# Kernel optimization log

Measured on AMD Instinct MI355X. Metric: run time of the kernel, lower is better.

The kernel has to match this reference:

```python
import jax, jax.numpy as jnp
import numpy as np

EMBED_DIM = 1024
NUM_HEADS = 16
HEAD_DIM = EMBED_DIM // NUM_HEADS
SCALE = HEAD_DIM ** -0.5


def setup_inputs() -> dict:
    key = jax.random.key(0)
    ks = jax.random.split(key, 5)
    B, N, D = 8, 1024, EMBED_DIM
    std = D ** -0.5
    x = jax.random.normal(ks[0], (B, N, D), dtype=jnp.float32)
    W_qkv = jax.random.normal(ks[1], (D, 3 * D), dtype=jnp.float32) * std
    b_qkv = jnp.zeros((3 * D,), dtype=jnp.float32)
    W_proj = jax.random.normal(ks[2], (D, D), dtype=jnp.float32) * std
    b_proj = jnp.zeros((D,), dtype=jnp.float32)
    return {"x": x, "W_qkv": W_qkv, "b_qkv": b_qkv, "W_proj": W_proj, "b_proj": b_proj}


def reference(x, W_qkv, b_qkv, W_proj, b_proj):
    B, N, D = x.shape
    H, hd = NUM_HEADS, HEAD_DIM
    # QKV projection: (B,N,3D) -> (3,B,H,N,hd)
    qkv = (x @ W_qkv + b_qkv).reshape(B, N, 3, H, hd).transpose(2, 0, 3, 1, 4)
    q, k, v = qkv[0], qkv[1], qkv[2]
    # scaled dot-product attention, full (B,H,N,N) scores as in original
    attn = jnp.einsum('bhqd,bhkd->bhqk', q, k) * SCALE
    attn = jax.nn.softmax(attn, axis=-1)
    out = jnp.einsum('bhqk,bhkd->bhqd', attn, v)  # (B,H,N,hd)
    out = out.transpose(0, 2, 1, 3).reshape(B, N, D)
    return out @ W_proj + b_proj
```

## Files before the change

### kernel.cpp

```cpp
#include <hip/hip_runtime.h>

#define AS1(p) ((const __attribute__((address_space(1))) void*)(p))
#define AS3(p) ((__attribute__((address_space(3))) void*)(p))

typedef __attribute__((ext_vector_type(8))) short bf16x8;
typedef __attribute__((ext_vector_type(4))) float f32x4;
typedef __attribute__((ext_vector_type(16))) float f32x16;

static constexpr int kBatch = 8;
static constexpr int kSeq = 1024;
static constexpr int kD = 1024;
static constexpr int kH = 16;
static constexpr int kHD = 64;
static constexpr int kRows = kBatch * kSeq;
static constexpr int kQKVCols = 3 * kD;

__device__ __forceinline__ unsigned short f2bf(float f) {
  union { float f; unsigned int u; } a; a.f = f;
  unsigned int r = a.u + 0x7fffu + ((a.u >> 16) & 1u);
  return (unsigned short)(r >> 16);
}

__device__ __forceinline__ unsigned pkbf(float a, float b) {
  unsigned r;
  asm("v_cvt_pk_bf16_f32 %0, %1, %2" : "=v"(r) : "v"(a), "v"(b));
  return r;
}

__global__ void cvt_bf16_kernel(const float* __restrict__ in,
                                unsigned short* __restrict__ out, int n4) {
  int i = blockIdx.x * blockDim.x + threadIdx.x;
  int stride = gridDim.x * blockDim.x;
  for (; i < n4; i += stride) {
    float4 v = reinterpret_cast<const float4*>(in)[i];
    ushort4 o;
    o.x = f2bf(v.x); o.y = f2bf(v.y); o.z = f2bf(v.z); o.w = f2bf(v.w);
    reinterpret_cast<ushort4*>(out)[i] = o;
  }
}

__global__ void transpose_cvt_kernel(const float* __restrict__ W,
                                     unsigned short* __restrict__ Wt,
                                     int rows, int cols) {
  __shared__ float tile[32][33];
  int c0 = blockIdx.x * 32, r0 = blockIdx.y * 32;
  int tx = threadIdx.x, ty = threadIdx.y;
#pragma unroll
  for (int i = 0; i < 32; i += 8)
    tile[ty + i][tx] = W[(size_t)(r0 + ty + i) * cols + (c0 + tx)];
  __syncthreads();
#pragma unroll
  for (int i = 0; i < 32; i += 8)
    Wt[(size_t)(c0 + ty + i) * rows + (r0 + tx)] = f2bf(tile[tx][ty + i]);
}

__device__ __forceinline__ int swap23(int x) {
  return (x & ~12) | ((x & 4) << 1) | ((x & 8) >> 1);
}
__global__ __launch_bounds__(256) void vtrans_kernel(
    const unsigned short* __restrict__ qkv, unsigned short* __restrict__ Vt) {
  __shared__ alignas(16) unsigned short tile[64][72];
  const int nt = blockIdx.x, bh = blockIdx.y;
  const int b = bh >> 4, h = bh & 15;
  const unsigned short* Vb = qkv + (size_t)b * kSeq * kQKVCols + 2 * kD + h * kHD;
  const int t = threadIdx.x;
#pragma unroll
  for (int r = 0; r < 2; ++r) {
    const int c = r * 256 + t;
    const int n = c >> 3, d8 = c & 7;
    uint4 v = *reinterpret_cast<const uint4*>(Vb + (size_t)(nt * 64 + n) * kQKVCols + d8 * 8);
    *reinterpret_cast<uint4*>(&tile[n][d8 * 8]) = v;
  }
  __syncthreads();
#pragma unroll
  for (int r = 0; r < 2; ++r) {
    const int c = r * 256 + t;
    const int d = c >> 3, n8 = c & 7;
    unsigned short w8[8];
#pragma unroll
    for (int j = 0; j < 8; ++j) w8[j] = tile[swap23(n8 * 8 + j)][d];
    *reinterpret_cast<uint4*>(Vt + (size_t)bh * kHD * kSeq + (size_t)d * kSeq + nt * 64 + n8 * 8) =
        *reinterpret_cast<uint4*>(w8);
  }
}

template <bool OUT_BF16>
__global__ __launch_bounds__(256) void gemm_bt_kernel(
    const unsigned short* __restrict__ A,
    const unsigned short* __restrict__ Bt,
    const float* __restrict__ bias,
    void* __restrict__ Cout, int M, int Nn, int K) {
  constexpr int BK = 64;
  __shared__ alignas(16) unsigned short As[128 * BK];
  __shared__ alignas(16) unsigned short Bs[128 * BK];
  const int t = threadIdx.x;
  const int lane = t & 63;
  const int w = t >> 6;
  const int wr = w >> 1, wc = w & 1;
  const int l15 = lane & 15, lhi = lane >> 4;
  const int nwg = gridDim.x * gridDim.y;
  const int lin = blockIdx.y * gridDim.x + blockIdx.x;
  const int swz = (lin & 7) * (nwg >> 3) + (lin >> 3);
  const int row0 = (swz / gridDim.x) * 128;
  const int col0 = (swz % gridDim.x) * 128;

  f32x4 acc[4][4] = {};
  const int ldsb = (t & ~63) * 16;

  for (int k0 = 0; k0 < K; k0 += BK) {
    __syncthreads();
#pragma unroll
    for (int r = 0; r < 4; ++r) {
      int c = r * 256 + t;
      int arow = c >> 3;
      int ccol = ((c & 7) ^ (arow & 7)) * 8;
      const unsigned short* ga = A + (size_t)(row0 + arow) * K + (k0 + ccol);
      const unsigned short* gb = Bt + (size_t)(col0 + arow) * K + (k0 + ccol);
      char* la = (char*)As + r * 4096 + ldsb;
      char* lb = (char*)Bs + r * 4096 + ldsb;
      __builtin_amdgcn_global_load_lds(AS1(ga), AS3(la), 16, 0, 0);
      __builtin_amdgcn_global_load_lds(AS1(gb), AS3(lb), 16, 0, 0);
    }
    __syncthreads();
#pragma unroll
    for (int kk = 0; kk < 2; ++kk) {
      bf16x8 af[4], bfr[4];
#pragma unroll
      for (int mi = 0; mi < 4; ++mi) {
        int rowa = wr * 64 + mi * 16 + l15;
        int chunk = (kk * 4 + lhi) ^ (rowa & 7);
        af[mi] = *reinterpret_cast<const bf16x8*>((const char*)As + rowa * 128 + chunk * 16);
      }
#pragma unroll
      for (int ni = 0; ni < 4; ++ni) {
        int rowb = wc * 64 + ni * 16 + l15;
        int chunk = (kk * 4 + lhi) ^ (rowb & 7);
        bfr[ni] = *reinterpret_cast<const bf16x8*>((const char*)Bs + rowb * 128 + chunk * 16);
      }
#pragma unroll
      for (int mi = 0; mi < 4; ++mi)
#pragma unroll
        for (int ni = 0; ni < 4; ++ni)
          acc[mi][ni] = __builtin_amdgcn_mfma_f32_16x16x32_bf16(af[mi], bfr[ni], acc[mi][ni], 0, 0, 0);
    }
  }
#pragma unroll
  for (int mi = 0; mi < 4; ++mi) {
    int rbase = row0 + wr * 64 + mi * 16 + lhi * 4;
#pragma unroll
    for (int ni = 0; ni < 4; ++ni) {
      int col = col0 + wc * 64 + ni * 16 + l15;
      float bv = bias[col];
#pragma unroll
      for (int j = 0; j < 4; ++j) {
        float v = acc[mi][ni][j] + bv;
        if (OUT_BF16)
          ((unsigned short*)Cout)[(size_t)(rbase + j) * Nn + col] = f2bf(v);
        else
          ((float*)Cout)[(size_t)(rbase + j) * Nn + col] = v;
      }
    }
  }
}

__global__ __launch_bounds__(256) void attn_kernel(
    const unsigned short* __restrict__ qkv,
    const unsigned short* __restrict__ Vt,
    unsigned short* __restrict__ ctx) {
  __shared__ alignas(16) char smem[32768];
  const int qt = blockIdx.x >> 7;
  const int bh = blockIdx.x & 127;
  const int b = bh >> 4, h = bh & 15;
  const int t = threadIdx.x, lane = t & 63, w = t >> 6;
  const int l31 = lane & 31, hi = lane >> 5;

  const unsigned short* Qb = qkv + (size_t)b * kSeq * kQKVCols + h * kHD;
  const unsigned short* Kb = Qb + kD;
  const unsigned short* Vtb = Vt + (size_t)bh * kHD * kSeq;

  bf16x8 qf[4];
  const int qrow = qt * 128 + w * 32 + l31;
#pragma unroll
  for (int s = 0; s < 4; ++s)
    qf[s] = *reinterpret_cast<const bf16x8*>(Qb + (size_t)qrow * kQKVCols + s * 16 + hi * 8);

  auto stage = [&](int kt, int bufb) {
#pragma unroll
    for (int r = 0; r < 2; ++r) {
      const int c = r * 256 + t;
      const int row = c >> 3;
      const int sc = ((c & 7) ^ (row & 7)) * 8;
      const unsigned short* gk = Kb + (size_t)(kt * 64 + row) * kQKVCols + sc;
      const unsigned short* gv = Vtb + (size_t)row * kSeq + kt * 64 + sc;
      char* lk = smem + bufb + r * 4096 + (t & ~63) * 16;
      char* lv = smem + bufb + 8192 + r * 4096 + (t & ~63) * 16;
      __builtin_amdgcn_global_load_lds(AS1(gk), AS3(lk), 16, 0, 0);
      __builtin_amdgcn_global_load_lds(AS1(gv), AS3(lv), 16, 0, 0);
    }
  };

  f32x16 oacc[2] = {};
  float mrun = -3.0e38f, lrun = 0.f;
  constexpr float kSc = 0.125f * 1.44269504f;

  stage(0, 0);
  __syncthreads();
  int cur = 0;
  for (int kt = 0; kt < 16; ++kt) {
    if (kt < 15) stage(kt + 1, (cur ^ 1) * 16384);
    const char* Kp = smem + cur * 16384;
    const char* Vp = Kp + 8192;

    f32x16 sacc[2] = {};
    __builtin_amdgcn_s_setprio(1);
#pragma unroll
    for (int nb = 0; nb < 2; ++nb) {
      const int n = nb * 32 + l31;
#pragma unroll
      for (int s = 0; s < 4; ++s) {
        const int ch = (s * 2 + hi) ^ (n & 7);
        bf16x8 kf = *reinterpret_cast<const bf16x8*>(Kp + n * 128 + ch * 16);
        sacc[nb] = __builtin_amdgcn_mfma_f32_32x32x16_bf16(kf, qf[s], sacc[nb], 0, 0, 0);
      }
    }
    __builtin_amdgcn_s_setprio(0);

    float tm = sacc[0][0];
#pragma unroll
    for (int nb = 0; nb < 2; ++nb)
#pragma unroll
      for (int r = 0; r < 16; ++r) tm = fmaxf(tm, sacc[nb][r]);
    tm = fmaxf(tm, __shfl_xor(tm, 32, 64));
    const float tms = tm * kSc;
    if (!__all(tms <= mrun + 8.0f)) {
      const float mnew = fmaxf(mrun, tms);
      const float corr = __builtin_amdgcn_exp2f(mrun - mnew);
      mrun = mnew;
      lrun *= corr;
#pragma unroll
      for (int db = 0; db < 2; ++db)
#pragma unroll
        for (int r = 0; r < 16; ++r) oacc[db][r] *= corr;
    }
    float ps = 0.f;
#pragma unroll
    for (int nb = 0; nb < 2; ++nb)
#pragma unroll
      for (int r = 0; r < 16; ++r) {
        const float e = __builtin_amdgcn_exp2f(__builtin_fmaf(sacc[nb][r], kSc, -mrun));
        sacc[nb][r] = e;
        ps += e;
      }
    lrun += ps + __shfl_xor(ps, 32, 64);

    bf16x8 pf[4];
#pragma unroll
    for (int s = 0; s < 4; ++s) {
      const int nb = s >> 1, h2 = (s & 1) * 8;
      union { unsigned u[4]; bf16x8 v; } pk4;
#pragma unroll
      for (int i = 0; i < 4; ++i)
        pk4.u[i] = pkbf(sacc[nb][h2 + 2 * i], sacc[nb][h2 + 2 * i + 1]);
      pf[s] = pk4.v;
    }

    __builtin_amdgcn_s_setprio(1);
#pragma unroll
    for (int db = 0; db < 2; ++db) {
      const int dr = db * 32 + l31;
#pragma unroll
      for (int s = 0; s < 4; ++s) {
        const int ch = (s * 2 + hi) ^ (dr & 7);
        bf16x8 vf = *reinterpret_cast<const bf16x8*>(Vp + dr * 128 + ch * 16);
        oacc[db] = __builtin_amdgcn_mfma_f32_32x32x16_bf16(vf, pf[s], oacc[db], 0, 0, 0);
      }
    }
    __builtin_amdgcn_s_setprio(0);
    __syncthreads();
    cur ^= 1;
  }

  const float rl = 1.0f / lrun;
  const int qlocal = w * 32 + l31;
#pragma unroll
  for (int db = 0; db < 2; ++db)
#pragma unroll
    for (int g = 0; g < 4; ++g) {
      const unsigned u0 = pkbf(oacc[db][g * 4 + 0] * rl, oacc[db][g * 4 + 1] * rl);
      const unsigned u1 = pkbf(oacc[db][g * 4 + 2] * rl, oacc[db][g * 4 + 3] * rl);
      const int ch = db * 4 + g;
      uint2 uu; uu.x = u0; uu.y = u1;
      *reinterpret_cast<uint2*>(smem + qlocal * 128 + ((ch ^ (qlocal & 7)) * 16) + hi * 8) = uu;
    }
  __syncthreads();
#pragma unroll
  for (int it = 0; it < 4; ++it) {
    const int idx = it * 256 + t;
    const int row = idx >> 3, ch = idx & 7;
    const uint4 vv = *reinterpret_cast<const uint4*>(smem + row * 128 + ((ch ^ (row & 7)) * 16));
    *reinterpret_cast<uint4*>(ctx + (size_t)(b * kSeq + qt * 128 + row) * kD + h * kHD + ch * 8) = vv;
  }
}

extern "C" void kernel_launch(void* const* d_in, const int* in_sizes, int n_in,
                              void* d_out, int out_size, void* d_ws, size_t ws_size,
                              hipStream_t stream) {
  const float* x     = (const float*)d_in[0];
  const float* Wqkv  = (const float*)d_in[1];
  const float* bqkv  = (const float*)d_in[2];
  const float* Wproj = (const float*)d_in[3];
  const float* bproj = (const float*)d_in[4];
  float* out = (float*)d_out;

  char* ws = (char*)d_ws;
  size_t oXbf   = 0;
  size_t oWqkvT = oXbf   + (size_t)kRows * kD * 2;
  size_t oWpT   = oWqkvT + (size_t)kQKVCols * kD * 2;
  size_t oQKV   = oWpT   + (size_t)kD * kD * 2;
  size_t oCTX   = oQKV   + (size_t)kRows * kQKVCols * 2;
  size_t total  = oCTX   + (size_t)kRows * kD * 2;
  if (ws_size < total) return;

  unsigned short* Xbf   = (unsigned short*)(ws + oXbf);
  unsigned short* Vtb   = (unsigned short*)(ws + oXbf);
  unsigned short* WqkvT = (unsigned short*)(ws + oWqkvT);
  unsigned short* WpT   = (unsigned short*)(ws + oWpT);
  unsigned short* QKV   = (unsigned short*)(ws + oQKV);
  unsigned short* CTX   = (unsigned short*)(ws + oCTX);

  cvt_bf16_kernel<<<2048, 256, 0, stream>>>(x, Xbf, kRows * kD / 4);
  transpose_cvt_kernel<<<dim3(kQKVCols / 32, kD / 32), dim3(32, 8), 0, stream>>>(Wqkv, WqkvT, kD, kQKVCols);
  transpose_cvt_kernel<<<dim3(kD / 32, kD / 32), dim3(32, 8), 0, stream>>>(Wproj, WpT, kD, kD);
  gemm_bt_kernel<true><<<dim3(kQKVCols / 128, kRows / 128), 256, 0, stream>>>(
      Xbf, WqkvT, bqkv, QKV, kRows, kQKVCols, kD);
  vtrans_kernel<<<dim3(16, 128), 256, 0, stream>>>(QKV, Vtb);
  attn_kernel<<<1024, 256, 0, stream>>>(QKV, Vtb, CTX);
  gemm_bt_kernel<false><<<dim3(kD / 128, kRows / 128), 256, 0, stream>>>(
      CTX, WpT, bproj, out, kRows, kD, kD);
}
```

Baseline: 168.8 us.

## Add 256x256-tile 8-wave pipelined GEMM for QKV projection

Result: no change. 170.1 us (+0.8%).

```diff
diff --git a/kernel.cpp b/kernel.cpp
--- a/kernel.cpp
+++ b/kernel.cpp
@@ -163,6 +163,137 @@
   }
 }
 
+#define G256_STAGE_A(BUF, HALF, KT)                                           \
+  do {                                                                        \
+    char* _d = smem + (BUF) * 65536 + (HALF) * 16384 + ldst;                  \
+    const unsigned short* _s0 = Ap + aoff0 + (size_t)(HALF) * halfstep + (KT) * 64; \
+    const unsigned short* _s1 = Ap + aoff1 + (size_t)(HALF) * halfstep + (KT) * 64; \
+    __builtin_amdgcn_global_load_lds(AS1(_s0), AS3(_d), 16, 0, 0);            \
+    __builtin_amdgcn_global_load_lds(AS1(_s1), AS3(_d + 8192), 16, 0, 0);     \
+  } while (0)
+#define G256_STAGE_B(BUF, HALF, KT)                                           \
+  do {                                                                        \
+    char* _d = smem + (BUF) * 65536 + 32768 + (HALF) * 16384 + ldst;          \
+    const unsigned short* _s0 = Bp + boff0 + (size_t)(HALF) * halfstep + (KT) * 64; \
+    const unsigned short* _s1 = Bp + boff1 + (size_t)(HALF) * halfstep + (KT) * 64; \
+    __builtin_amdgcn_global_load_lds(AS1(_s0), AS3(_d), 16, 0, 0);            \
+    __builtin_amdgcn_global_load_lds(AS1(_s1), AS3(_d + 8192), 16, 0, 0);     \
+  } while (0)
+#define G256_PHASE(RBUF, QM, QN, STAGE_STMT, DO_VM)                           \
+  do {                                                                        \
+    const char* _Ab = smem + (RBUF) * 65536 + (QM) * 16384;                   \
+    const char* _Bb = smem + (RBUF) * 65536 + 32768 + (QN) * 16384;           \
+    bf16x8 _af[2][4], _bf[2][2];                                              \
+    _Pragma("unroll") for (int kk = 0; kk < 2; ++kk) {                        \
+      _Pragma("unroll") for (int mi = 0; mi < 4; ++mi) {                      \
+        const int rr = wm * 64 + mi * 16 + l15;                               \
+        const int ch = (kk * 4 + lhi) ^ (rr & 7);                             \
+        _af[kk][mi] = *reinterpret_cast<const bf16x8*>(_Ab + rr * 128 + ch * 16); \
+      }                                                                       \
+      _Pragma("unroll") for (int ni = 0; ni < 2; ++ni) {                      \
+        const int rr = wn * 32 + ni * 16 + l15;                               \
+        const int ch = (kk * 4 + lhi) ^ (rr & 7);                             \
+        _bf[kk][ni] = *reinterpret_cast<const bf16x8*>(_Bb + rr * 128 + ch * 16); \
+      }                                                                       \
+    }                                                                         \
+    STAGE_STMT;                                                               \
+    if (DO_VM) asm volatile("s_waitcnt vmcnt(4)" ::: "memory");               \
+    asm volatile("" ::: "memory");                                            \
+    __builtin_amdgcn_s_barrier();                                             \
+    asm volatile("s_waitcnt lgkmcnt(0)" ::: "memory");                        \
+    __builtin_amdgcn_sched_barrier(0);                                        \
+    __builtin_amdgcn_s_setprio(1);                                            \
+    _Pragma("unroll") for (int kk = 0; kk < 2; ++kk)                          \
+      _Pragma("unroll") for (int mi = 0; mi < 4; ++mi)                        \
+        _Pragma("unroll") for (int ni = 0; ni < 2; ++ni)                      \
+          acc[QM][QN][mi][ni] = __builtin_amdgcn_mfma_f32_16x16x32_bf16(      \
+              _af[kk][mi], _bf[kk][ni], acc[QM][QN][mi][ni], 0, 0, 0);        \
+    __builtin_amdgcn_s_setprio(0);                                            \
+    asm volatile("" ::: "memory");                                            \
+    __builtin_amdgcn_s_barrier();                                             \
+    asm volatile("" ::: "memory");                                            \
+  } while (0)
+
+template <bool OUT_BF16>
+__global__ __launch_bounds__(512, 2) void gemm256_kernel(
+    const unsigned short* __restrict__ Ap,
+    const unsigned short* __restrict__ Bp,
+    const float* __restrict__ bias,
+    void* __restrict__ Cout, int M, int Nn, int K) {
+  __shared__ alignas(16) char smem[131072];
+  const int t = threadIdx.x;
+  const int lane = t & 63;
+  const int wid = t >> 6;
+  const int wm = wid >> 2, wn = wid & 3;
+  const int l15 = lane & 15, lhi = lane >> 4;
+
+  const int nwg = gridDim.x * gridDim.y;
+  const int lin = blockIdx.y * gridDim.x + blockIdx.x;
+  const int swz = (lin & 7) * (nwg >> 3) + (lin >> 3);
+  const int row0 = (swz / gridDim.x) * 256;
+  const int col0 = (swz % gridDim.x) * 256;
+
+  const int r0i = t >> 3, r1i = (512 + t) >> 3;
+  const int sc0 = ((t & 7) ^ (r0i & 7)) * 8;
+  const int sc1 = (((512 + t) & 7) ^ (r1i & 7)) * 8;
+  const size_t aoff0 = (size_t)(row0 + r0i) * K + sc0;
+  const size_t aoff1 = (size_t)(row0 + r1i) * K + sc1;
+  const size_t boff0 = (size_t)(col0 + r0i) * K + sc0;
+  const size_t boff1 = (size_t)(col0 + r1i) * K + sc1;
+  const size_t halfstep = (size_t)128 * K;
+  const int ldst = (t & ~63) * 16;
+
+  f32x4 acc[2][2][4][2] = {};
+
+  G256_STAGE_A(0, 0, 0);
+  G256_STAGE_B(0, 1, 0);
+  G256_STAGE_A(0, 1, 0);
+  G256_STAGE_B(0, 0, 0);
+  G256_STAGE_A(1, 0, 1);
+  G256_STAGE_B(1, 1, 1);
+  asm volatile("s_waitcnt vmcnt(4)" ::: "memory");
+  __builtin_amdgcn_s_barrier();
+  asm volatile("" ::: "memory");
+
+  const int nkt = K >> 6;
+  const int niter = nkt >> 1;
+  for (int i = 0; i < niter; ++i) {
+    const int tc1 = 2 * i + 1;
+    const int tn0 = (2 * i + 2) & (nkt - 1);
+    const int tn1 = (2 * i + 3) & (nkt - 1);
+    G256_PHASE(0, 0, 0, G256_STAGE_A(1, 1, tc1), 0);
+    G256_PHASE(0, 0, 1, G256_STAGE_B(1, 0, tc1), 0);
+    G256_PHASE(0, 1, 1, G256_STAGE_A(0, 0, tn0), 0);
+    G256_PHASE(0, 1, 0, G256_STAGE_B(0, 1, tn0), 1);
+    G256_PHASE(1, 0, 0, G256_STAGE_A(0, 1, tn0), 0);
+    G256_PHASE(1, 0, 1, G256_STAGE_B(0, 0, tn0), 0);
+    G256_PHASE(1, 1, 1, G256_STAGE_A(1, 0, tn1), 0);
+    G256_PHASE(1, 1, 0, G256_STAGE_B(1, 1, tn1), 1);
+  }
+
+#pragma unroll
+  for (int qm = 0; qm < 2; ++qm)
+#pragma unroll
+    for (int mi = 0; mi < 4; ++mi) {
+      const int rbase = row0 + qm * 128 + wm * 64 + mi * 16 + lhi * 4;
+#pragma unroll
+      for (int qn = 0; qn < 2; ++qn)
+#pragma unroll
+        for (int ni = 0; ni < 2; ++ni) {
+          const int col = col0 + qn * 128 + wn * 32 + ni * 16 + l15;
+          const float bv = bias[col];
+#pragma unroll
+          for (int j = 0; j < 4; ++j) {
+            const float v = acc[qm][qn][mi][ni][j] + bv;
+            if (OUT_BF16)
+              ((unsigned short*)Cout)[(size_t)(rbase + j) * Nn + col] = f2bf(v);
+            else
+              ((float*)Cout)[(size_t)(rbase + j) * Nn + col] = v;
+          }
+        }
+    }
+}
+
 __global__ __launch_bounds__(256) void attn_kernel(
     const unsigned short* __restrict__ qkv,
     const unsigned short* __restrict__ Vt,
@@ -331,7 +462,7 @@
   cvt_bf16_kernel<<<2048, 256, 0, stream>>>(x, Xbf, kRows * kD / 4);
   transpose_cvt_kernel<<<dim3(kQKVCols / 32, kD / 32), dim3(32, 8), 0, stream>>>(Wqkv, WqkvT, kD, kQKVCols);
   transpose_cvt_kernel<<<dim3(kD / 32, kD / 32), dim3(32, 8), 0, stream>>>(Wproj, WpT, kD, kD);
-  gemm_bt_kernel<true><<<dim3(kQKVCols / 128, kRows / 128), 256, 0, stream>>>(
+  gemm256_kernel<true><<<dim3(kQKVCols / 256, kRows / 256), 512, 0, stream>>>(
       Xbf, WqkvT, bqkv, QKV, kRows, kQKVCols, kD);
   vtrans_kernel<<<dim3(16, 128), 256, 0, stream>>>(QKV, Vtb);
   attn_kernel<<<1024, 256, 0, stream>>>(QKV, Vtb, CTX);
```

## Fuse prep kernels into one launch and write transposed V from QKV GEMM epilogue

Applied to the files above, without the earlier changes.

Measured after the change: 161.1 us. -4.5%, faster.

```diff
diff --git a/kernel.cpp b/kernel.cpp
--- a/kernel.cpp
+++ b/kernel.cpp
@@ -27,36 +27,48 @@
   return r;
 }
 
-__global__ void cvt_bf16_kernel(const float* __restrict__ in,
-                                unsigned short* __restrict__ out, int n4) {
-  int i = blockIdx.x * blockDim.x + threadIdx.x;
-  int stride = gridDim.x * blockDim.x;
-  for (; i < n4; i += stride) {
-    float4 v = reinterpret_cast<const float4*>(in)[i];
-    ushort4 o;
-    o.x = f2bf(v.x); o.y = f2bf(v.y); o.z = f2bf(v.z); o.w = f2bf(v.w);
-    reinterpret_cast<ushort4*>(out)[i] = o;
-  }
-}
-
-__global__ void transpose_cvt_kernel(const float* __restrict__ W,
-                                     unsigned short* __restrict__ Wt,
-                                     int rows, int cols) {
+__device__ __forceinline__ int swap23(int x) {
+  return (x & ~12) | ((x & 4) << 1) | ((x & 8) >> 1);
+}
+
+__global__ __launch_bounds__(256) void prep_kernel(
+    const float* __restrict__ x, unsigned short* __restrict__ Xbf,
+    const float* __restrict__ Wqkv, unsigned short* __restrict__ WqkvT,
+    const float* __restrict__ Wproj, unsigned short* __restrict__ WpT) {
+  const int bid = blockIdx.x, t = threadIdx.x;
+  if (bid < 1024) {
+    const int n4 = kRows * kD / 4;
+    int i = bid * 256 + t;
+    const int stride = 1024 * 256;
+    for (; i < n4; i += stride) {
+      float4 v = reinterpret_cast<const float4*>(x)[i];
+      ushort4 o;
+      o.x = f2bf(v.x); o.y = f2bf(v.y); o.z = f2bf(v.z); o.w = f2bf(v.w);
+      reinterpret_cast<ushort4*>(Xbf)[i] = o;
+    }
+    return;
+  }
   __shared__ float tile[32][33];
-  int c0 = blockIdx.x * 32, r0 = blockIdx.y * 32;
-  int tx = threadIdx.x, ty = threadIdx.y;
+  const float* W; unsigned short* Wt; int cols, c0, r0;
+  if (bid < 4096) {
+    const int idx = bid - 1024;
+    W = Wqkv; Wt = WqkvT; cols = kQKVCols;
+    c0 = (idx % 96) * 32; r0 = (idx / 96) * 32;
+  } else {
+    const int idx = bid - 4096;
+    W = Wproj; Wt = WpT; cols = kD;
+    c0 = (idx % 32) * 32; r0 = (idx / 32) * 32;
+  }
+  const int tx = t & 31, ty = t >> 5;
 #pragma unroll
   for (int i = 0; i < 32; i += 8)
     tile[ty + i][tx] = W[(size_t)(r0 + ty + i) * cols + (c0 + tx)];
   __syncthreads();
 #pragma unroll
   for (int i = 0; i < 32; i += 8)
-    Wt[(size_t)(c0 + ty + i) * rows + (r0 + tx)] = f2bf(tile[tx][ty + i]);
-}
-
-__device__ __forceinline__ int swap23(int x) {
-  return (x & ~12) | ((x & 4) << 1) | ((x & 8) >> 1);
-}
+    Wt[(size_t)(c0 + ty + i) * 1024 + (r0 + tx)] = f2bf(tile[tx][ty + i]);
+}
+
 __global__ __launch_bounds__(256) void vtrans_kernel(
     const unsigned short* __restrict__ qkv, unsigned short* __restrict__ Vt) {
   __shared__ alignas(16) unsigned short tile[64][72];
@@ -84,12 +96,13 @@
   }
 }
 
-template <bool OUT_BF16>
+template <int MODE>
 __global__ __launch_bounds__(256) void gemm_bt_kernel(
     const unsigned short* __restrict__ A,
     const unsigned short* __restrict__ Bt,
     const float* __restrict__ bias,
-    void* __restrict__ Cout, int M, int Nn, int K) {
+    void* __restrict__ Cout, unsigned short* __restrict__ Vt,
+    int M, int Nn, int K) {
   constexpr int BK = 64;
   __shared__ alignas(16) unsigned short As[128 * BK];
   __shared__ alignas(16) unsigned short Bs[128 * BK];
@@ -144,6 +157,28 @@
           acc[mi][ni] = __builtin_amdgcn_mfma_f32_16x16x32_bf16(af[mi], bfr[ni], acc[mi][ni], 0, 0, 0);
     }
   }
+
+  if (MODE == 2 && col0 >= 2048) {
+#pragma unroll
+    for (int mi = 0; mi < 4; ++mi) {
+      const int rbase = row0 + wr * 64 + mi * 16 + lhi * 4;
+      const int b = rbase >> 10, n = rbase & 1023;
+      const int nbase = (n & ~63) | swap23(n & 63);
+#pragma unroll
+      for (int ni = 0; ni < 4; ++ni) {
+        const int col = col0 + wc * 64 + ni * 16 + l15;
+        const int hv = (col >> 6) - 32;
+        const int d = col & 63;
+        const float bv = bias[col];
+        uint2 uu;
+        uu.x = pkbf(acc[mi][ni][0] + bv, acc[mi][ni][1] + bv);
+        uu.y = pkbf(acc[mi][ni][2] + bv, acc[mi][ni][3] + bv);
+        *reinterpret_cast<uint2*>(Vt + ((size_t)((b << 4) + hv) << 16) + d * 1024 + nbase) = uu;
+      }
+    }
+    return;
+  }
+
 #pragma unroll
   for (int mi = 0; mi < 4; ++mi) {
     int rbase = row0 + wr * 64 + mi * 16 + lhi * 4;
@@ -154,7 +189,7 @@
 #pragma unroll
       for (int j = 0; j < 4; ++j) {
         float v = acc[mi][ni][j] + bv;
-        if (OUT_BF16)
+        if (MODE != 0)
           ((unsigned short*)Cout)[(size_t)(rbase + j) * Nn + col] = f2bf(v);
         else
           ((float*)Cout)[(size_t)(rbase + j) * Nn + col] = v;
@@ -318,23 +353,31 @@
   size_t oWpT   = oWqkvT + (size_t)kQKVCols * kD * 2;
   size_t oQKV   = oWpT   + (size_t)kD * kD * 2;
   size_t oCTX   = oQKV   + (size_t)kRows * kQKVCols * 2;
-  size_t total  = oCTX   + (size_t)kRows * kD * 2;
-  if (ws_size < total) return;
+  size_t oVt    = oCTX   + (size_t)kRows * kD * 2;
+  size_t total_base  = oVt;
+  size_t total_fused = oVt + (size_t)kRows * kD * 2;
+  if (ws_size < total_base) return;
+  const bool fused_vt = ws_size >= total_fused;
 
   unsigned short* Xbf   = (unsigned short*)(ws + oXbf);
-  unsigned short* Vtb   = (unsigned short*)(ws + oXbf);
   unsigned short* WqkvT = (unsigned short*)(ws + oWqkvT);
   unsigned short* WpT   = (unsigned short*)(ws + oWpT);
   unsigned short* QKV   = (unsigned short*)(ws + oQKV);
   unsigned short* CTX   = (unsigned short*)(ws + oCTX);
-
-  cvt_bf16_kernel<<<2048, 256, 0, stream>>>(x, Xbf, kRows * kD / 4);
-  transpose_cvt_kernel<<<dim3(kQKVCols / 32, kD / 32), dim3(32, 8), 0, stream>>>(Wqkv, WqkvT, kD, kQKVCols);
-  transpose_cvt_kernel<<<dim3(kD / 32, kD / 32), dim3(32, 8), 0, stream>>>(Wproj, WpT, kD, kD);
-  gemm_bt_kernel<true><<<dim3(kQKVCols / 128, kRows / 128), 256, 0, stream>>>(
-      Xbf, WqkvT, bqkv, QKV, kRows, kQKVCols, kD);
-  vtrans_kernel<<<dim3(16, 128), 256, 0, stream>>>(QKV, Vtb);
-  attn_kernel<<<1024, 256, 0, stream>>>(QKV, Vtb, CTX);
-  gemm_bt_kernel<false><<<dim3(kD / 128, kRows / 128), 256, 0, stream>>>(
-      CTX, WpT, bproj, out, kRows, kD, kD);
-}
+  unsigned short* VtF   = (unsigned short*)(ws + oVt);
+  unsigned short* VtA   = (unsigned short*)(ws + oXbf);
+
+  prep_kernel<<<5120, 256, 0, stream>>>(x, Xbf, Wqkv, WqkvT, Wproj, WpT);
+  if (fused_vt) {
+    gemm_bt_kernel<2><<<dim3(kQKVCols / 128, kRows / 128), 256, 0, stream>>>(
+        Xbf, WqkvT, bqkv, QKV, VtF, kRows, kQKVCols, kD);
+    attn_kernel<<<1024, 256, 0, stream>>>(QKV, VtF, CTX);
+  } else {
+    gemm_bt_kernel<1><<<dim3(kQKVCols / 128, kRows / 128), 256, 0, stream>>>(
+        Xbf, WqkvT, bqkv, QKV, nullptr, kRows, kQKVCols, kD);
+    vtrans_kernel<<<dim3(16, 128), 256, 0, stream>>>(QKV, VtA);
+    attn_kernel<<<1024, 256, 0, stream>>>(QKV, VtA, CTX);
+  }
+  gemm_bt_kernel<0><<<dim3(kD / 128, kRows / 128), 256, 0, stream>>>(
+      CTX, WpT, bproj, out, nullptr, kRows, kD, kD);
+}
```
